# Performance work log

Hardware: AMD Instinct MI355X
Metric: run time of the kernel (lower is better)

Reference implementation:

```python
import jax, jax.numpy as jnp
import numpy as np


def setup_inputs() -> dict:
    key = jax.random.key(0)
    k1, k2 = jax.random.split(key)
    B, N, M, D = 8, 8192, 8192, 3
    gts = jax.random.normal(k1, (B, N, D), dtype=jnp.float32)
    preds = jax.random.normal(k2, (B, M, D), dtype=jnp.float32)
    return {"gts": gts, "preds": preds}


def reference(gts, preds):
    # Chamfer distance (pytorch3d defaults): squared L2, mean over points,
    # mean over batch, sum of both directions.
    x2 = jnp.sum(gts * gts, axis=-1)          # [B, N]
    y2 = jnp.sum(preds * preds, axis=-1)      # [B, M]
    xy = jnp.einsum('bnd,bmd->bnm', gts, preds)  # [B, N, M]
    d2 = x2[:, :, None] + y2[:, None, :] - 2.0 * xy
    d2 = jnp.maximum(d2, 0.0)  # guard tiny negative values from cancellation
    cham_x = jnp.mean(jnp.min(d2, axis=2))  # x -> nearest y, mean over N then B
    cham_y = jnp.mean(jnp.min(d2, axis=1))  # y -> nearest x, mean over M then B
    return cham_x + cham_y
```

## Files before the change

### kernel.cpp

```cpp
#include <hip/hip_runtime.h>
#include <hip/hip_bf16.h>
#include <math.h>


#define BLOCK 256
#define WAVES 4
#define QPW 64

typedef short short8 __attribute__((ext_vector_type(8)));
typedef float f32x16 __attribute__((ext_vector_type(16)));

__device__ __forceinline__ unsigned int bf16hi(float f) {
    __hip_bfloat16 h = __float2bfloat16(f);
    return (unsigned int)*reinterpret_cast<unsigned short*>(&h);
}
__device__ __forceinline__ float bf16f(unsigned int u) {
    unsigned int v = u << 16;
    return *reinterpret_cast<float*>(&v);
}
__device__ __forceinline__ void cvt_split(float v, unsigned int& hi, unsigned int& lo) {
    hi = bf16hi(v);
    lo = bf16hi(v - bf16f(hi));
}

#define MFMA(a, b, c) __builtin_amdgcn_mfma_f32_32x32x16_bf16((a), (b), (c), 0, 0, 0)

__global__ void prep_kernel(const float* __restrict__ gts, const float* __restrict__ preds,
                            int nG, int nP, unsigned char* __restrict__ recB) {
    const int idx = blockIdx.x * blockDim.x + threadIdx.x;
    if (idx >= nG + nP) return;
    const float* src;
    unsigned char* rb;
    if (idx < nG) {
        src = gts + 3 * (size_t)idx;
        rb  = recB + (size_t)(idx >> 5) * 1024 + (size_t)(idx & 31) * 16;
    } else {
        const int j = idx - nG;
        src = preds + 3 * (size_t)j;
        rb  = recB + (size_t)nG * 32 + (size_t)(j >> 5) * 1024 + (size_t)(j & 31) * 16;
    }
    const float x = src[0], y = src[1], z = src[2];
    const float w = -0.5f * (x * x + y * y + z * z);
    unsigned int xh, xl, yh, yl, zh, zl, wh, wl;
    cvt_split(x, xh, xl); cvt_split(y, yh, yl);
    cvt_split(z, zh, zl); cvt_split(w, wh, wl);
    const unsigned int hx = xh | (yh << 16), hz = zh | (wh << 16);
    const unsigned int lx = xl | (yl << 16), lz = zl | (wl << 16);
    *(uint4*)(rb)       = make_uint4(hx, hz, hx, hz);
    *(uint4*)(rb + 512) = make_uint4(lx, lz, 0u, 0u);
}

__global__ void __launch_bounds__(BLOCK, 2)
chamfer_kernel(const float* __restrict__ gts, const float* __restrict__ preds,
               const uint4* __restrict__ recB, int N, int M, int B,
               float invx, float invy, float* __restrict__ out) {
    const int z = blockIdx.y;
    const bool dirX = (z < B);
    const int b = dirX ? z : z - B;
    const int NQ = dirX ? N : M;
    const int NR = dirX ? M : N;
    const float* Q = (dirX ? gts : preds) + (size_t)b * NQ * 3;
    const float inv = dirX ? invx : invy;
    const uint4* Rb4 = recB + (dirX ? (size_t)B * N * 2 : 0) + (size_t)b * NR * 2;

    const int tid = threadIdx.x;
    const int lane = tid & 63;
    const int wave = tid >> 6;
    const int m = lane & 31;
    const bool isHi = lane < 32;
    const unsigned int loMask = isHi ? 0xFFFFFFFFu : 0u;
    const int qBase = (blockIdx.x * WAVES + wave) * QPW;

    float n2q0, n2q1;
    short8 A0, A1;
    {
        const float* qp = Q + 3 * (size_t)(qBase + m);
        const float x = qp[0], y = qp[1], zz = qp[2];
        n2q0 = x * x + y * y + zz * zz;
        unsigned int xh, xl, yh, yl, zh, zl;
        cvt_split(x, xh, xl); cvt_split(y, yh, yl); cvt_split(zz, zh, zl);
        uint4 a = make_uint4(xh | (yh << 16), zh | 0x3F800000u,
                             (xl | (yl << 16)) & loMask, zl & loMask);
        A0 = __builtin_bit_cast(short8, a);
    }
    {
        const float* qp = Q + 3 * (size_t)(qBase + 32 + m);
        const float x = qp[0], y = qp[1], zz = qp[2];
        n2q1 = x * x + y * y + zz * zz;
        unsigned int xh, xl, yh, yl, zh, zl;
        cvt_split(x, xh, xl); cvt_split(y, yh, yl); cvt_split(zz, zh, zl);
        uint4 a = make_uint4(xh | (yh << 16), zh | 0x3F800000u,
                             (xl | (yl << 16)) & loMask, zl & loMask);
        A1 = __builtin_bit_cast(short8, a);
    }

    f32x16 k0, k1, zc;
    #pragma unroll
    for (int r = 0; r < 16; ++r) { k0[r] = -INFINITY; k1[r] = -INFINITY; zc[r] = 0.0f; }

#define DO2(ba, bb) do {                                                     \
        const short8 sa_ = __builtin_bit_cast(short8, (ba));                 \
        const short8 sb_ = __builtin_bit_cast(short8, (bb));                 \
        const f32x16 c0_ = MFMA(A0, sa_, zc);                                \
        const f32x16 c1_ = MFMA(A0, sb_, zc);                                \
        const f32x16 c2_ = MFMA(A1, sa_, zc);                                \
        const f32x16 c3_ = MFMA(A1, sb_, zc);                                \
        _Pragma("unroll")                                                    \
        for (int r = 0; r < 16; ++r)                                         \
            k0[r] = fmaxf(fmaxf(c0_[r], c1_[r]), k0[r]);                     \
        _Pragma("unroll")                                                    \
        for (int r = 0; r < 16; ++r)                                         \
            k1[r] = fmaxf(fmaxf(c2_[r], c3_[r]), k1[r]);                     \
    } while (0)

    const int NT = NR / 32;
    const uint4* p = Rb4 + lane;
    uint4 S0 = p[0], S1 = p[64], S2 = p[128], S3 = p[192];
    #pragma unroll 1
    for (int g = 0; g < NT / 4; g += 2) {
        const uint4* pT = p + 256;
        const uint4 T0 = pT[0], T1 = pT[64], T2 = pT[128], T3 = pT[192];
        DO2(S0, S1); DO2(S2, S3);
        const uint4* pS = p + 512;
        S0 = pS[0]; S1 = pS[64]; S2 = pS[128]; S3 = pS[192];
        DO2(T0, T1); DO2(T2, T3);
        p += 512;
    }
#undef DO2

    __shared__ float sT[WAVES][64][36];
    #pragma unroll
    for (int r = 0; r < 16; ++r) {
        const int row = (r & 3) + 8 * (r >> 2) + 4 * (lane >> 5);
        sT[wave][row][m]      = k0[r];
        sT[wave][32 + row][m] = k1[r];
    }
    const float4* rowp = (const float4*)&sT[wave][lane][0];
    float4 m01 = rowp[0];
    #pragma unroll
    for (int kk = 1; kk < 8; ++kk) {
        const float4 t = rowp[kk];
        m01.x = fmaxf(m01.x, t.x); m01.y = fmaxf(m01.y, t.y);
        m01.z = fmaxf(m01.z, t.z); m01.w = fmaxf(m01.w, t.w);
    }
    const float cmax = fmaxf(fmaxf(m01.x, m01.y), fmaxf(m01.z, m01.w));

    const float q2own = isHi ? n2q0 : n2q1;
    float v = fmaxf(q2own - 2.0f * cmax, 0.0f) * inv;

    #pragma unroll
    for (int off = 32; off; off >>= 1) v += __shfl_xor(v, off);
    __shared__ float waveSums[WAVES];
    if (lane == 0) waveSums[wave] = v;
    __syncthreads();
    if (tid == 0) {
        float s = 0.0f;
        #pragma unroll
        for (int w = 0; w < WAVES; ++w) s += waveSums[w];
        atomicAdd(out, s);
    }
}

extern "C" void kernel_launch(void* const* d_in, const int* in_sizes, int n_in,
                              void* d_out, int out_size, void* d_ws, size_t ws_size,
                              hipStream_t stream) {
    const float* gts   = (const float*)d_in[0];
    const float* preds = (const float*)d_in[1];
    float* out = (float*)d_out;

    const int B = 8;
    const int N = in_sizes[0] / (B * 3);
    const int M = in_sizes[1] / (B * 3);
    const int nG = B * N, nP = B * M;

    unsigned char* recB = (unsigned char*)d_ws;

    prep_kernel<<<(nG + nP + BLOCK - 1) / BLOCK, BLOCK, 0, stream>>>(
        gts, preds, nG, nP, recB);

    dim3 grid(N / (WAVES * QPW), 2 * B);
    chamfer_kernel<<<grid, BLOCK, 0, stream>>>(
        gts, preds, (const uint4*)recB, N, M, B,
        1.0f / (float)nG, 1.0f / (float)nP, out);
}
```

Baseline: 96.55 us.

## Halve queries per wave to one MFMA tile and raise occupancy

Each wave now handles 32 query points (one A fragment) instead of 64, so each reference B fragment loaded feeds two MFMAs instead of four. The accumulator and register footprint roughly halves, launch bounds go up to 4 blocks per CU, the grid doubles, and the prefetch pipeline is restructured around pairs of tiles. The epilogue reduction is adapted to split each row across two half-waves with a cross-lane shuffle. The cost is twice the reference-stream loads per query, which lowers arithmetic intensity in exchange for more latency hiding from extra waves.

```diff
diff --git a/kernel.cpp b/kernel.cpp
--- a/kernel.cpp
+++ b/kernel.cpp
@@ -5,7 +5,7 @@
 
 #define BLOCK 256
 #define WAVES 4
-#define QPW 64
+#define QPW 32
 
 typedef short short8 __attribute__((ext_vector_type(8)));
 typedef float f32x16 __attribute__((ext_vector_type(16)));
@@ -50,7 +50,7 @@
     *(uint4*)(rb + 512) = make_uint4(lx, lz, 0u, 0u);
 }
 
-__global__ void __launch_bounds__(BLOCK, 2)
+__global__ void __launch_bounds__(BLOCK, 4)
 chamfer_kernel(const float* __restrict__ gts, const float* __restrict__ preds,
                const uint4* __restrict__ recB, int N, int M, int B,
                float invx, float invy, float* __restrict__ out) {
@@ -71,82 +71,66 @@
     const unsigned int loMask = isHi ? 0xFFFFFFFFu : 0u;
     const int qBase = (blockIdx.x * WAVES + wave) * QPW;
 
-    float n2q0, n2q1;
-    short8 A0, A1;
+    float n2q;
+    short8 A0;
     {
         const float* qp = Q + 3 * (size_t)(qBase + m);
         const float x = qp[0], y = qp[1], zz = qp[2];
-        n2q0 = x * x + y * y + zz * zz;
+        n2q = x * x + y * y + zz * zz;
         unsigned int xh, xl, yh, yl, zh, zl;
         cvt_split(x, xh, xl); cvt_split(y, yh, yl); cvt_split(zz, zh, zl);
         uint4 a = make_uint4(xh | (yh << 16), zh | 0x3F800000u,
                              (xl | (yl << 16)) & loMask, zl & loMask);
         A0 = __builtin_bit_cast(short8, a);
     }
-    {
-        const float* qp = Q + 3 * (size_t)(qBase + 32 + m);
-        const float x = qp[0], y = qp[1], zz = qp[2];
-        n2q1 = x * x + y * y + zz * zz;
-        unsigned int xh, xl, yh, yl, zh, zl;
-        cvt_split(x, xh, xl); cvt_split(y, yh, yl); cvt_split(zz, zh, zl);
-        uint4 a = make_uint4(xh | (yh << 16), zh | 0x3F800000u,
-                             (xl | (yl << 16)) & loMask, zl & loMask);
-        A1 = __builtin_bit_cast(short8, a);
-    }
 
-    f32x16 k0, k1, zc;
+    f32x16 k0, zc;
     #pragma unroll
-    for (int r = 0; r < 16; ++r) { k0[r] = -INFINITY; k1[r] = -INFINITY; zc[r] = 0.0f; }
+    for (int r = 0; r < 16; ++r) { k0[r] = -INFINITY; zc[r] = 0.0f; }
 
 #define DO2(ba, bb) do {                                                     \
         const short8 sa_ = __builtin_bit_cast(short8, (ba));                 \
         const short8 sb_ = __builtin_bit_cast(short8, (bb));                 \
         const f32x16 c0_ = MFMA(A0, sa_, zc);                                \
         const f32x16 c1_ = MFMA(A0, sb_, zc);                                \
-        const f32x16 c2_ = MFMA(A1, sa_, zc);                                \
-        const f32x16 c3_ = MFMA(A1, sb_, zc);                                \
         _Pragma("unroll")                                                    \
         for (int r = 0; r < 16; ++r)                                         \
             k0[r] = fmaxf(fmaxf(c0_[r], c1_[r]), k0[r]);                     \
-        _Pragma("unroll")                                                    \
-        for (int r = 0; r < 16; ++r)                                         \
-            k1[r] = fmaxf(fmaxf(c2_[r], c3_[r]), k1[r]);                     \
     } while (0)
 
     const int NT = NR / 32;
     const uint4* p = Rb4 + lane;
-    uint4 S0 = p[0], S1 = p[64], S2 = p[128], S3 = p[192];
+    uint4 S0 = p[0], S1 = p[64];
+    uint4 T0 = p[128], T1 = p[192];
     #pragma unroll 1
-    for (int g = 0; g < NT / 4; g += 2) {
-        const uint4* pT = p + 256;
-        const uint4 T0 = pT[0], T1 = pT[64], T2 = pT[128], T3 = pT[192];
-        DO2(S0, S1); DO2(S2, S3);
-        const uint4* pS = p + 512;
-        S0 = pS[0]; S1 = pS[64]; S2 = pS[128]; S3 = pS[192];
-        DO2(T0, T1); DO2(T2, T3);
-        p += 512;
+    for (int t = 0; t < NT; t += 4) {
+        const uint4 nS0 = p[256], nS1 = p[320];
+        DO2(S0, S1);
+        const uint4 nT0 = p[384], nT1 = p[448];
+        DO2(T0, T1);
+        S0 = nS0; S1 = nS1; T0 = nT0; T1 = nT1;
+        p += 256;
     }
 #undef DO2
 
-    __shared__ float sT[WAVES][64][36];
+    __shared__ float sT[WAVES][32][36];
     #pragma unroll
     for (int r = 0; r < 16; ++r) {
         const int row = (r & 3) + 8 * (r >> 2) + 4 * (lane >> 5);
-        sT[wave][row][m]      = k0[r];
-        sT[wave][32 + row][m] = k1[r];
+        sT[wave][row][m] = k0[r];
     }
-    const float4* rowp = (const float4*)&sT[wave][lane][0];
+    const float4* rowp = (const float4*)&sT[wave][lane & 31][(lane >> 5) * 16];
     float4 m01 = rowp[0];
     #pragma unroll
-    for (int kk = 1; kk < 8; ++kk) {
+    for (int kk = 1; kk < 4; ++kk) {
         const float4 t = rowp[kk];
         m01.x = fmaxf(m01.x, t.x); m01.y = fmaxf(m01.y, t.y);
         m01.z = fmaxf(m01.z, t.z); m01.w = fmaxf(m01.w, t.w);
     }
-    const float cmax = fmaxf(fmaxf(m01.x, m01.y), fmaxf(m01.z, m01.w));
+    float rmax = fmaxf(fmaxf(m01.x, m01.y), fmaxf(m01.z, m01.w));
+    rmax = fmaxf(rmax, __shfl_xor(rmax, 32));
 
-    const float q2own = isHi ? n2q0 : n2q1;
-    float v = fmaxf(q2own - 2.0f * cmax, 0.0f) * inv;
+    float v = isHi ? fmaxf(n2q - 2.0f * rmax, 0.0f) * inv : 0.0f;
 
     #pragma unroll
     for (int off = 32; off; off >>= 1) v += __shfl_xor(v, off);
```

Measured after the change: 105.5 us. 9.2% more time.

## Software-pipeline MFMA issue with max-fold of previous tile results

Applied to the files above, without the earlier changes.

Restructures the main loop so the four MFMAs for the next pair of reference tiles are issued before the fmax reduction of the previous tile's results, using two ping-pong accumulator sets. Loads are prefetched eight tiles deep in a rotating register buffer. The goal is to hide MFMA latency behind the VALU max-folding instead of stalling on each result. In exchange it costs more live vector registers, and the final iterations prefetch past the end of the batch's tile stream and compute one unused MFMA set.

```diff
diff --git a/kernel.cpp b/kernel.cpp
--- a/kernel.cpp
+++ b/kernel.cpp
@@ -24,6 +24,7 @@
 }
 
 #define MFMA(a, b, c) __builtin_amdgcn_mfma_f32_32x32x16_bf16((a), (b), (c), 0, 0, 0)
+#define BC8(x) __builtin_bit_cast(short8, (x))
 
 __global__ void prep_kernel(const float* __restrict__ gts, const float* __restrict__ preds,
                             int nG, int nP, unsigned char* __restrict__ recB) {
@@ -81,7 +82,7 @@
         cvt_split(x, xh, xl); cvt_split(y, yh, yl); cvt_split(zz, zh, zl);
         uint4 a = make_uint4(xh | (yh << 16), zh | 0x3F800000u,
                              (xl | (yl << 16)) & loMask, zl & loMask);
-        A0 = __builtin_bit_cast(short8, a);
+        A0 = BC8(a);
     }
     {
         const float* qp = Q + 3 * (size_t)(qBase + 32 + m);
@@ -91,42 +92,50 @@
         cvt_split(x, xh, xl); cvt_split(y, yh, yl); cvt_split(zz, zh, zl);
         uint4 a = make_uint4(xh | (yh << 16), zh | 0x3F800000u,
                              (xl | (yl << 16)) & loMask, zl & loMask);
-        A1 = __builtin_bit_cast(short8, a);
+        A1 = BC8(a);
     }
 
     f32x16 k0, k1, zc;
     #pragma unroll
     for (int r = 0; r < 16; ++r) { k0[r] = -INFINITY; k1[r] = -INFINITY; zc[r] = 0.0f; }
 
-#define DO2(ba, bb) do {                                                     \
-        const short8 sa_ = __builtin_bit_cast(short8, (ba));                 \
-        const short8 sb_ = __builtin_bit_cast(short8, (bb));                 \
-        const f32x16 c0_ = MFMA(A0, sa_, zc);                                \
-        const f32x16 c1_ = MFMA(A0, sb_, zc);                                \
-        const f32x16 c2_ = MFMA(A1, sa_, zc);                                \
-        const f32x16 c3_ = MFMA(A1, sb_, zc);                                \
+    f32x16 cA0, cA1, cA2, cA3, cB0, cB1, cB2, cB3;
+
+#define MF4(P, ba, bb) do {                                                  \
+        P##0 = MFMA(A0, BC8(ba), zc);                                        \
+        P##1 = MFMA(A0, BC8(bb), zc);                                        \
+        P##2 = MFMA(A1, BC8(ba), zc);                                        \
+        P##3 = MFMA(A1, BC8(bb), zc);                                        \
+    } while (0)
+#define FOLD(P) do {                                                         \
         _Pragma("unroll")                                                    \
         for (int r = 0; r < 16; ++r)                                         \
-            k0[r] = fmaxf(fmaxf(c0_[r], c1_[r]), k0[r]);                     \
+            k0[r] = fmaxf(fmaxf(P##0[r], P##1[r]), k0[r]);                   \
         _Pragma("unroll")                                                    \
         for (int r = 0; r < 16; ++r)                                         \
-            k1[r] = fmaxf(fmaxf(c2_[r], c3_[r]), k1[r]);                     \
+            k1[r] = fmaxf(fmaxf(P##2[r], P##3[r]), k1[r]);                   \
     } while (0)
 
     const int NT = NR / 32;
     const uint4* p = Rb4 + lane;
-    uint4 S0 = p[0], S1 = p[64], S2 = p[128], S3 = p[192];
+    uint4 X0 = p[0],   X1 = p[64],  X2 = p[128], X3 = p[192];
+    uint4 X4 = p[256], X5 = p[320], X6 = p[384], X7 = p[448];
+    MF4(cA, X0, X1);
+
     #pragma unroll 1
-    for (int g = 0; g < NT / 4; g += 2) {
-        const uint4* pT = p + 256;
-        const uint4 T0 = pT[0], T1 = pT[64], T2 = pT[128], T3 = pT[192];
-        DO2(S0, S1); DO2(S2, S3);
-        const uint4* pS = p + 512;
-        S0 = pS[0]; S1 = pS[64]; S2 = pS[128]; S3 = pS[192];
-        DO2(T0, T1); DO2(T2, T3);
+    for (int bdy = 0; bdy < NT / 8; ++bdy) {
+        X0 = p[512]; X1 = p[576];
+        MF4(cB, X2, X3);  FOLD(cA);
+        X2 = p[640]; X3 = p[704];
+        MF4(cA, X4, X5);  FOLD(cB);
+        X4 = p[768]; X5 = p[832];
+        MF4(cB, X6, X7);  FOLD(cA);
+        X6 = p[896]; X7 = p[960];
+        MF4(cA, X0, X1);  FOLD(cB);
         p += 512;
     }
-#undef DO2
+#undef MF4
+#undef FOLD
 
     __shared__ float sT[WAVES][64][36];
     #pragma unroll
@@ -174,7 +183,6 @@
     const int nG = B * N, nP = B * M;
 
     unsigned char* recB = (unsigned char*)d_ws;
-
     prep_kernel<<<(nG + nP + BLOCK - 1) / BLOCK, BLOCK, 0, stream>>>(
         gts, preds, nG, nP, recB);
 
```

Result: slower. 100.7 us (+4.3%).
